# Optimization experiments

Measured on AMD Instinct MI355X. Metric: run time of the kernel, lower is better.

## Reference

```python
import jax, jax.numpy as jnp
import numpy as np

N, E, D_IN, H, L = 50000, 1_600_000, 3, 128, 4
MASK_RATIO = 0.15
GAMMA = 2.0
BN_EPS = 1e-5


def setup_inputs() -> dict:
    key = jax.random.key(0)
    ks = jax.random.split(key, 16)
    inp = {
        "x": jax.random.normal(ks[0], (N, D_IN), dtype=jnp.float32),
        "edge_index": jax.random.randint(ks[1], (2, E), 0, N, dtype=jnp.int32),
        "edge_attr": jax.random.normal(ks[2], (E, 4), dtype=jnp.float32),
        "mask": jax.random.uniform(ks[3], (N,)) < MASK_RATIO,
        # learned parameters
        "mask_token": 0.02 * jax.random.normal(ks[4], (D_IN,), dtype=jnp.float32),
        "embed_W": 0.1 * jax.random.normal(ks[5], (D_IN, H), dtype=jnp.float32),
        "embed_b": jnp.zeros((H,), dtype=jnp.float32),
        "conv_W1": 0.05 * jax.random.normal(ks[6], (L, H, 2 * H), dtype=jnp.float32),
        "conv_b1": jnp.zeros((L, 2 * H), dtype=jnp.float32),
        "conv_W2": 0.05 * jax.random.normal(ks[7], (L, 2 * H, H), dtype=jnp.float32),
        "conv_b2": jnp.zeros((L, H), dtype=jnp.float32),
        "bn_gamma": jnp.ones((L, H), dtype=jnp.float32),
        "bn_beta": jnp.zeros((L, H), dtype=jnp.float32),
        "dec_W1": 0.05 * jax.random.normal(ks[8], (H, H), dtype=jnp.float32),
        "dec_b1": jnp.zeros((H,), dtype=jnp.float32),
        "dec_W2": 0.05 * jax.random.normal(ks[9], (H, D_IN), dtype=jnp.float32),
        "dec_b2": jnp.zeros((D_IN,), dtype=jnp.float32),
    }
    return inp


def _l2norm(v):
    n = jnp.linalg.norm(v, axis=-1, keepdims=True)
    return v / jnp.maximum(n, 1e-12)


def reference(x, edge_index, edge_attr, mask, mask_token, embed_W, embed_b,
              conv_W1, conv_b1, conv_W2, conv_b2, bn_gamma, bn_beta,
              dec_W1, dec_b1, dec_W2, dec_b2):
    # --- masking: replace masked node features with learnable mask token ---
    masked_x = jnp.where(mask[:, None], mask_token[None, :], x)

    # --- GIN encoder ---
    h = masked_x @ embed_W + embed_b  # [N, H]
    src, dst = edge_index[0], edge_index[1]
    for l in range(L):
        # scatter-add aggregation: sum_{j in N(i)} h_j  (GINConv, eps=0)
        agg = jax.ops.segment_sum(h[src], dst, num_segments=N)  # [N, H]
        z = agg + h
        # MLP: H -> 2H -> H with ReLU
        z = jax.nn.relu(z @ conv_W1[l] + conv_b1[l]) @ conv_W2[l] + conv_b2[l]
        # BatchNorm1d (training-mode batch statistics, biased variance)
        mean = jnp.mean(z, axis=0)
        var = jnp.mean(jnp.square(z - mean), axis=0)
        z = (z - mean) * jax.lax.rsqrt(var + BN_EPS) * bn_gamma[l] + bn_beta[l]
        h = jax.nn.relu(z)  # dropout = identity (eval)

    # --- decoder: H -> H -> D_IN ---
    recon = jax.nn.relu(h @ dec_W1 + dec_b1) @ dec_W2 + dec_b2  # [N, D_IN]

    # --- scaled cosine error over masked nodes ---
    cos = jnp.sum(_l2norm(recon) * _l2norm(x), axis=-1)  # [N]
    per_node = jnp.power(1.0 - cos, GAMMA)
    m = mask.astype(recon.dtype)
    loss = jnp.sum(per_node * m) / jnp.maximum(jnp.sum(m), 1.0)
    return loss, recon
```

## Files before the change

### kernel.cpp

```cpp
#include <hip/hip_runtime.h>
#include <cstdint>

#define N_NODES 50000
#define N_EDGES 1600000
#define HDIM 128
#define L_LAYERS 4
#define BN_EPS 1e-5f
#define NPART 196
#define PART_SHIFT 8
#define PB_CHUNK 6250
#define FP_CAP 16384
#define FL_RB 128

typedef __attribute__((ext_vector_type(8))) short short8v;
typedef __attribute__((ext_vector_type(4))) float f32x4;

__device__ __forceinline__ unsigned short f2bf(float f) {
    uint32_t u = __builtin_bit_cast(uint32_t, f);
    u += 0x7fff + ((u >> 16) & 1);
    return (unsigned short)(u >> 16);
}
__device__ __forceinline__ float bf2f(unsigned short b) {
    return __builtin_bit_cast(float, (uint32_t)b << 16);
}

__global__ void detect_mask_kernel(const uint32_t* __restrict__ mw, int* __restrict__ flag) {
    __shared__ int f;
    if (threadIdx.x == 0) f = 0;
    __syncthreads();
    int found = 0;
    for (int i = threadIdx.x; i < 12500; i += blockDim.x)
        if (mw[i] > 1u) found = 1;
    if (found) f = 1;
    __syncthreads();
    if (threadIdx.x == 0) *flag = f;
}

__device__ __forceinline__ int read_mask(const void* mask, int i, int bytelayout) {
    if (bytelayout) return ((const unsigned char*)mask)[i] != 0;
    return ((const int*)mask)[i] != 0;
}

__global__ void wprep_all_kernel(const float* __restrict__ W1, const float* __restrict__ W2,
                                 const float* __restrict__ dW1, unsigned short* __restrict__ Wt1,
                                 unsigned short* __restrict__ Wt2,
                                 unsigned short* __restrict__ Wtd) {
    int seg = blockIdx.y;
    const float* W;
    unsigned short* Wt;
    int K, nshift;
    if (seg < 4) {
        W = W1 + (size_t)seg * HDIM * 2 * HDIM;
        Wt = Wt1 + (size_t)seg * HDIM * 2 * HDIM;
        K = HDIM;
        nshift = 8;
    } else if (seg < 8) {
        int l = seg - 4;
        W = W2 + (size_t)l * 2 * HDIM * HDIM;
        Wt = Wt2 + (size_t)l * 2 * HDIM * HDIM;
        K = 2 * HDIM;
        nshift = 7;
    } else {
        W = dW1;
        Wt = Wtd;
        K = HDIM;
        nshift = 7;
    }
    int total = K << nshift;
    for (int idx = blockIdx.x * 256 + threadIdx.x; idx < total; idx += gridDim.x * 256) {
        int k = idx >> nshift, n = idx & ((1 << nshift) - 1);
        Wt[(size_t)n * K + k] = f2bf(W[idx]);
    }
}

__global__ void embed_kernel(const float* __restrict__ x, const void* __restrict__ mask,
                             const int* __restrict__ flag, const float* __restrict__ tok,
                             const float* __restrict__ W, const float* __restrict__ b,
                             unsigned short* __restrict__ h) {
    int idx = blockIdx.x * blockDim.x + threadIdx.x;
    if (idx >= N_NODES * HDIM) return;
    int i = idx >> 7, c = idx & 127;
    int fl = *flag;
    int m = read_mask(mask, i, fl);
    float x0 = m ? tok[0] : x[i * 3 + 0];
    float x1 = m ? tok[1] : x[i * 3 + 1];
    float x2 = m ? tok[2] : x[i * 3 + 2];
    h[idx] = f2bf(x0 * W[c] + x1 * W[HDIM + c] + x2 * W[2 * HDIM + c] + b[c]);
}

__global__ __launch_bounds__(256) void pcount_kernel(const int* __restrict__ dst,
                                                     int* __restrict__ pcount) {
    __shared__ int hist[NPART];
    for (int i = threadIdx.x; i < NPART; i += 256) hist[i] = 0;
    __syncthreads();
    int lo = blockIdx.x * PB_CHUNK;
    for (int i = threadIdx.x; i < PB_CHUNK; i += 256)
        atomicAdd(&hist[dst[lo + i] >> PART_SHIFT], 1);
    __syncthreads();
    for (int i = threadIdx.x; i < NPART; i += 256)
        if (hist[i]) atomicAdd(&pcount[i], hist[i]);
}

__global__ __launch_bounds__(256) void pscan_kernel(const int* __restrict__ pcount,
                                                    int* __restrict__ poff,
                                                    int* __restrict__ pcursor,
                                                    int* __restrict__ rowptr) {
    __shared__ int sh[256];
    int t = threadIdx.x;
    int v = (t < NPART) ? pcount[t] : 0;
    sh[t] = v;
    __syncthreads();
    for (int o = 1; o < 256; o <<= 1) {
        int u = (t >= o) ? sh[t - o] : 0;
        __syncthreads();
        sh[t] += u;
        __syncthreads();
    }
    if (t < NPART) {
        int e = sh[t] - v;
        poff[t] = e;
        pcursor[t] = e;
    }
    if (t == NPART - 1) {
        poff[NPART] = sh[t];
        rowptr[N_NODES] = sh[t];
    }
}

__global__ __launch_bounds__(256) void partition_kernel(const int* __restrict__ src,
                                                        const int* __restrict__ dst,
                                                        int* __restrict__ pcursor,
                                                        uint32_t* __restrict__ pairs) {
    __shared__ int hist[NPART];
    __shared__ int off[NPART];
    int b = blockIdx.x, t = threadIdx.x;
    int lo = b * PB_CHUNK;
    for (int i = t; i < NPART; i += 256) hist[i] = 0;
    __syncthreads();
    for (int i = t; i < PB_CHUNK; i += 256) {
        int d = dst[lo + i];
        atomicAdd(&hist[d >> PART_SHIFT], 1);
    }
    __syncthreads();
    for (int i = t; i < NPART; i += 256) off[i] = atomicAdd(&pcursor[i], hist[i]);
    __syncthreads();
    for (int i = t; i < PB_CHUNK; i += 256) {
        int d = dst[lo + i];
        int s = src[lo + i];
        int pos = atomicAdd(&off[d >> PART_SHIFT], 1);
        pairs[pos] = (uint32_t)s | ((uint32_t)(d & 255) << 16);
    }
}

__global__ __launch_bounds__(256) void fill_part_kernel(const uint32_t* __restrict__ pairs,
                                                        const int* __restrict__ poff,
                                                        int* __restrict__ rowptr,
                                                        int* __restrict__ col) {
    __shared__ int colw[FP_CAP];
    __shared__ int lscan[256];
    __shared__ int lcur[256];
    int p = blockIdx.x, t = threadIdx.x;
    int base = p << PART_SHIFT;
    int nlocal = min(256, N_NODES - base);
    int pstart = poff[p], pend = poff[p + 1];
    int cnt = pend - pstart;
    lcur[t] = 0;
    __syncthreads();
    for (int e = pstart + t; e < pend; e += 256)
        atomicAdd(&lcur[(__builtin_nontemporal_load(&pairs[e]) >> 16) & 255], 1);
    __syncthreads();
    int v = lcur[t];
    lscan[t] = v;
    __syncthreads();
    for (int o = 1; o < 256; o <<= 1) {
        int u = (t >= o) ? lscan[t - o] : 0;
        __syncthreads();
        lscan[t] += u;
        __syncthreads();
    }
    int excl = lscan[t] - v;
    if (t < nlocal) rowptr[base + t] = pstart + excl;
    lcur[t] = excl;
    __syncthreads();
    if (cnt <= FP_CAP) {
        for (int e = pstart + t; e < pend; e += 256) {
            uint32_t pv = pairs[e];
            int pos = atomicAdd(&lcur[(pv >> 16) & 255], 1);
            colw[pos] = (int)(pv & 0xFFFFu);
        }
        __syncthreads();
        for (int e = t; e < cnt; e += 256) col[pstart + e] = colw[e];
    } else {
        for (int e = pstart + t; e < pend; e += 256) {
            uint32_t pv = pairs[e];
            int pos = atomicAdd(&lcur[(pv >> 16) & 255], 1);
            col[pstart + pos] = (int)(pv & 0xFFFFu);
        }
    }
}

__global__ __launch_bounds__(256) void agg_kernel(const unsigned short* __restrict__ h,
                                                  const int* __restrict__ rowptr,
                                                  const int* __restrict__ col,
                                                  unsigned short* __restrict__ z) {
    int wid = threadIdx.x >> 6;
    int lane = threadIdx.x & 63;
    int i = blockIdx.x * 4 + wid;
    if (i >= N_NODES) return;
    int start = rowptr[i], end = rowptr[i + 1];
    const uint32_t* h32 = (const uint32_t*)h;
    uint32_t u = h32[(size_t)i * 64 + lane];
    float ax = __builtin_bit_cast(float, u << 16);
    float ay = __builtin_bit_cast(float, u & 0xffff0000u);
    float bx = 0.f, by = 0.f, cx = 0.f, cy = 0.f, dx = 0.f, dy = 0.f;
    int e = start;
    for (; e + 4 <= end; e += 4) {
        int j0 = col[e + 0], j1 = col[e + 1], j2 = col[e + 2], j3 = col[e + 3];
        uint32_t u0 = h32[(size_t)j0 * 64 + lane];
        uint32_t u1 = h32[(size_t)j1 * 64 + lane];
        uint32_t u2 = h32[(size_t)j2 * 64 + lane];
        uint32_t u3 = h32[(size_t)j3 * 64 + lane];
        ax += __builtin_bit_cast(float, u0 << 16);
        ay += __builtin_bit_cast(float, u0 & 0xffff0000u);
        bx += __builtin_bit_cast(float, u1 << 16);
        by += __builtin_bit_cast(float, u1 & 0xffff0000u);
        cx += __builtin_bit_cast(float, u2 << 16);
        cy += __builtin_bit_cast(float, u2 & 0xffff0000u);
        dx += __builtin_bit_cast(float, u3 << 16);
        dy += __builtin_bit_cast(float, u3 & 0xffff0000u);
    }
    for (; e < end; ++e) {
        uint32_t u0 = h32[(size_t)col[e] * 64 + lane];
        ax += __builtin_bit_cast(float, u0 << 16);
        ay += __builtin_bit_cast(float, u0 & 0xffff0000u);
    }
    ax += bx + cx + dx;
    ay += by + cy + dy;
    uint32_t o = (uint32_t)f2bf(ax) | ((uint32_t)f2bf(ay) << 16);
    ((uint32_t*)z)[(size_t)i * 64 + lane] = o;
}

__global__ __launch_bounds__(512) void fused_layer_kernel(
    const unsigned short* __restrict__ z, const unsigned short* __restrict__ Wt1,
    const float* __restrict__ b1, const unsigned short* __restrict__ Wt2,
    const float* __restrict__ b2, float* __restrict__ zin, float* __restrict__ stats, int M) {
    __shared__ unsigned short wbuf[256 * 136];
    __shared__ unsigned short z1l[FL_RB * 264];
    const int t = threadIdx.x;
    const int lane = t & 63;
    const int w = t >> 6;
    const int r = lane & 15, ks = lane >> 4;
    const int row0 = blockIdx.x * FL_RB + w * 16;
    const int arow = min(row0 + r, M - 1);
    for (int i = t; i < 256 * 16; i += 512) {
        int row = i >> 4, seg = i & 15;
        *(short8v*)&wbuf[row * 136 + seg * 8] = *(const short8v*)&Wt1[(size_t)row * 128 + seg * 8];
    }
    short8v a4[4];
#pragma unroll
    for (int kk = 0; kk < 4; ++kk)
        a4[kk] = *(const short8v*)&z[(size_t)arow * HDIM + kk * 32 + ks * 8];
    __syncthreads();
#pragma unroll
    for (int n = 0; n < 16; ++n) {
        f32x4 acc = (f32x4){0.f, 0.f, 0.f, 0.f};
#pragma unroll
        for (int kk = 0; kk < 4; ++kk) {
            short8v bf = *(const short8v*)&wbuf[(n * 16 + r) * 136 + kk * 32 + ks * 8];
            acc = __builtin_amdgcn_mfma_f32_16x16x32_bf16(a4[kk], bf, acc, 0, 0, 0);
        }
        float bv = b1[n * 16 + r];
#pragma unroll
        for (int i = 0; i < 4; ++i) {
            float o = fmaxf(acc[i] + bv, 0.f);
            z1l[(w * 16 + ks * 4 + i) * 264 + n * 16 + r] = f2bf(o);
        }
    }
    __syncthreads();
    for (int i = t; i < 128 * 32; i += 512) {
        int row = i >> 5, seg = i & 31;
        *(short8v*)&wbuf[row * 264 + seg * 8] = *(const short8v*)&Wt2[(size_t)row * 256 + seg * 8];
    }
    __syncthreads();
    f32x4 accb[8];
#pragma unroll
    for (int n = 0; n < 8; ++n) accb[n] = (f32x4){0.f, 0.f, 0.f, 0.f};
#pragma unroll
    for (int k0 = 0; k0 < 256; k0 += 32) {
        short8v a = *(const short8v*)&z1l[(w * 16 + r) * 264 + k0 + ks * 8];
#pragma unroll
        for (int n = 0; n < 8; ++n) {
            short8v bf = *(const short8v*)&wbuf[(n * 16 + r) * 264 + k0 + ks * 8];
            accb[n] = __builtin_amdgcn_mfma_f32_16x16x32_bf16(a, bf, accb[n], 0, 0, 0);
        }
    }
    __syncthreads();
    float* sred = (float*)wbuf;
#pragma unroll
    for (int n = 0; n < 8; ++n) {
        const int cc = n * 16 + r;
        const float bv = b2[cc];
        float s = 0.f, ss = 0.f;
#pragma unroll
        for (int i = 0; i < 4; ++i) {
            int row = row0 + ks * 4 + i;
            if (row < M) {
                float o = accb[n][i] + bv;
                s += o;
                ss += o * o;
                zin[(size_t)row * HDIM + cc] = o;
            }
        }
        s += __shfl_xor(s, 16);
        s += __shfl_xor(s, 32);
        ss += __shfl_xor(ss, 16);
        ss += __shfl_xor(ss, 32);
        if (ks == 0) {
            sred[(w * 2 + 0) * HDIM + cc] = s;
            sred[(w * 2 + 1) * HDIM + cc] = ss;
        }
    }
    __syncthreads();
    if (t < HDIM) {
        float s = 0.f, ss = 0.f;
#pragma unroll
        for (int ww = 0; ww < 8; ++ww) {
            s += sred[(ww * 2 + 0) * HDIM + t];
            ss += sred[(ww * 2 + 1) * HDIM + t];
        }
        atomicAdd(&stats[t], s);
        atomicAdd(&stats[HDIM + t], ss);
    }
}

template <int K, bool OUT_BF16, bool RELU>
__global__ __launch_bounds__(256) void mfma_gemm_kernel(const unsigned short* __restrict__ A,
                                                        const unsigned short* __restrict__ Wt,
                                                        const float* __restrict__ bias,
                                                        void* __restrict__ C, int M, int ldc) {
    const int lane = threadIdx.x & 63;
    const int w = threadIdx.x >> 6;
    const int row0 = blockIdx.y * 64 + w * 16;
    const int col0 = blockIdx.x * 64;
    const int r = lane & 15;
    const int ks = lane >> 4;
    const int arow = min(row0 + r, M - 1);
    f32x4 acc[4];
#pragma unroll
    for (int n = 0; n < 4; ++n) acc[n] = (f32x4){0.f, 0.f, 0.f, 0.f};
#pragma unroll
    for (int k0 = 0; k0 < K; k0 += 32) {
        short8v a = *(const short8v*)&A[(size_t)arow * K + k0 + ks * 8];
#pragma unroll
        for (int n = 0; n < 4; ++n) {
            short8v b = *(const short8v*)&Wt[(size_t)(col0 + n * 16 + r) * K + k0 + ks * 8];
            acc[n] = __builtin_amdgcn_mfma_f32_16x16x32_bf16(a, b, acc[n], 0, 0, 0);
        }
    }
#pragma unroll
    for (int n = 0; n < 4; ++n) {
        const int col = col0 + n * 16 + r;
        const float bv = bias[col];
#pragma unroll
        for (int i = 0; i < 4; ++i) {
            int row = row0 + ks * 4 + i;
            if (row < M) {
                float o = acc[n][i] + bv;
                if (RELU) o = fmaxf(o, 0.f);
                if (OUT_BF16)
                    ((unsigned short*)C)[(size_t)row * ldc + col] = f2bf(o);
                else
                    ((float*)C)[(size_t)row * ldc + col] = o;
            }
        }
    }
}

__global__ void bnapply_kernel(const float* __restrict__ zin, const float* __restrict__ stats,
                               const float* __restrict__ gamma, const float* __restrict__ beta,
                               unsigned short* __restrict__ h) {
    __shared__ float ssc[2 * HDIM];
    int t = threadIdx.x;
    if (t < HDIM) {
        float mean = stats[t] * (1.f / N_NODES);
        float var = stats[HDIM + t] * (1.f / N_NODES) - mean * mean;
        float rstd = rsqrtf(fmaxf(var, 0.f) + BN_EPS);
        float s = gamma[t] * rstd;
        ssc[t] = s;
        ssc[HDIM + t] = beta[t] - mean * s;
    }
    __syncthreads();
    int idx = blockIdx.x * blockDim.x + threadIdx.x;
    if (idx >= N_NODES * HDIM / 4) return;
    float4 v = ((const float4*)zin)[idx];
    int c = (idx * 4) & 127;
    float o0 = fmaxf(v.x * ssc[c + 0] + ssc[HDIM + c + 0], 0.f);
    float o1 = fmaxf(v.y * ssc[c + 1] + ssc[HDIM + c + 1], 0.f);
    float o2 = fmaxf(v.z * ssc[c + 2] + ssc[HDIM + c + 2], 0.f);
    float o3 = fmaxf(v.w * ssc[c + 3] + ssc[HDIM + c + 3], 0.f);
    uint2 p;
    p.x = (uint32_t)f2bf(o0) | ((uint32_t)f2bf(o1) << 16);
    p.y = (uint32_t)f2bf(o2) | ((uint32_t)f2bf(o3) << 16);
    ((uint2*)h)[idx] = p;
}

__global__ __launch_bounds__(256) void dec2_loss_kernel(
    const unsigned short* __restrict__ d1, const float* __restrict__ W2,
    const float* __restrict__ b2, const float* __restrict__ x, const void* __restrict__ mask,
    const int* __restrict__ flag, float* __restrict__ recon, float* __restrict__ acc) {
    __shared__ float w2s[HDIM * 3];
    for (int t = threadIdx.x; t < HDIM * 3; t += 256) w2s[t] = W2[t];
    __syncthreads();
    int i = blockIdx.x * 256 + threadIdx.x;
    int fl = *flag;
    float lsum = 0.f, lcnt = 0.f;
    if (i < N_NODES) {
        float s0 = 0.f, s1 = 0.f, s2 = 0.f;
        const unsigned short* row = &d1[(size_t)i * HDIM];
#pragma unroll
        for (int k0 = 0; k0 < HDIM; k0 += 8) {
            short8v v = *(const short8v*)&row[k0];
#pragma unroll
            for (int q = 0; q < 8; ++q) {
                float a = bf2f((unsigned short)v[q]);
                s0 = fmaf(a, w2s[(k0 + q) * 3 + 0], s0);
                s1 = fmaf(a, w2s[(k0 + q) * 3 + 1], s1);
                s2 = fmaf(a, w2s[(k0 + q) * 3 + 2], s2);
            }
        }
        float r0 = s0 + b2[0], r1 = s1 + b2[1], r2 = s2 + b2[2];
        recon[(size_t)i * 3 + 0] = r0;
        recon[(size_t)i * 3 + 1] = r1;
        recon[(size_t)i * 3 + 2] = r2;
        if (read_mask(mask, i, fl)) {
            float rn = fmaxf(sqrtf(r0 * r0 + r1 * r1 + r2 * r2), 1e-12f);
            float x0 = x[i * 3 + 0], x1 = x[i * 3 + 1], x2 = x[i * 3 + 2];
            float xn = fmaxf(sqrtf(x0 * x0 + x1 * x1 + x2 * x2), 1e-12f);
            float cs = (r0 * x0 + r1 * x1 + r2 * x2) / (rn * xn);
            float d = 1.f - cs;
            lsum = d * d;
            lcnt = 1.f;
        }
    }
#pragma unroll
    for (int o = 32; o > 0; o >>= 1) {
        lsum += __shfl_xor(lsum, o);
        lcnt += __shfl_xor(lcnt, o);
    }
    if ((threadIdx.x & 63) == 0 && lcnt != 0.f) {
        atomicAdd(&acc[0], lsum);
        atomicAdd(&acc[1], lcnt);
    }
}

__global__ void finalize_kernel(const float* __restrict__ acc, float* __restrict__ out) {
    out[0] = acc[0] / fmaxf(acc[1], 1.f);
}

extern "C" void kernel_launch(void* const* d_in, const int* in_sizes, int n_in, void* d_out,
                              int out_size, void* d_ws, size_t ws_size, hipStream_t stream) {
    const float* x = (const float*)d_in[0];
    const int* ei = (const int*)d_in[1];
    const int* src = ei;
    const int* dst = ei + N_EDGES;
    const void* mask = d_in[3];
    const float* tok = (const float*)d_in[4];
    const float* eW = (const float*)d_in[5];
    const float* eb = (const float*)d_in[6];
    const float* W1 = (const float*)d_in[7];
    const float* b1 = (const float*)d_in[8];
    const float* W2 = (const float*)d_in[9];
    const float* b2 = (const float*)d_in[10];
    const float* gm = (const float*)d_in[11];
    const float* bt = (const float*)d_in[12];
    const float* dW1 = (const float*)d_in[13];
    const float* db1 = (const float*)d_in[14];
    const float* dW2 = (const float*)d_in[15];
    const float* db2 = (const float*)d_in[16];
    float* out = (float*)d_out;

    char* ws = (char*)d_ws;
    size_t off = 0;
    auto alloc = [&](size_t bytes) -> void* {
        void* p = ws + off;
        off = (off + bytes + 255) & ~(size_t)255;
        return p;
    };
    unsigned short* h = (unsigned short*)alloc((size_t)N_NODES * HDIM * 2);
    unsigned short* z = (unsigned short*)alloc((size_t)N_NODES * HDIM * 2);
    unsigned short* z1 = (unsigned short*)alloc((size_t)N_NODES * 2 * HDIM * 2);
    float* zin = (float*)alloc((size_t)N_NODES * HDIM * 4);
    unsigned short* Wt1 = (unsigned short*)alloc((size_t)L_LAYERS * HDIM * 2 * HDIM * 2);
    unsigned short* Wt2 = (unsigned short*)alloc((size_t)L_LAYERS * HDIM * 2 * HDIM * 2);
    unsigned short* Wtd = (unsigned short*)alloc((size_t)HDIM * HDIM * 2);
    int* rowptr = (int*)alloc((size_t)(N_NODES + 1) * 4);
    int* col = (int*)alloc((size_t)N_EDGES * 4);
    uint32_t* pairs = (uint32_t*)alloc((size_t)N_EDGES * 4);
    int* pcount = (int*)alloc((size_t)NPART * 4);
    int* poff = (int*)alloc((size_t)(NPART + 1) * 4);
    int* pcursor = (int*)alloc((size_t)NPART * 4);
    float* stats = (float*)alloc((size_t)L_LAYERS * 2 * HDIM * 4);
    float* lacc = (float*)alloc(8);
    int* flag = (int*)alloc(4);

    detect_mask_kernel<<<1, 256, 0, stream>>>((const uint32_t*)mask, flag);
    wprep_all_kernel<<<dim3(32, 9), 256, 0, stream>>>(W1, W2, dW1, Wt1, Wt2, Wtd);
    embed_kernel<<<(N_NODES * HDIM + 255) / 256, 256, 0, stream>>>(x, mask, flag, tok, eW, eb, h);

    hipMemsetAsync(pcount, 0, (size_t)NPART * 4, stream);
    hipMemsetAsync(stats, 0, (size_t)L_LAYERS * 2 * HDIM * 4, stream);
    hipMemsetAsync(lacc, 0, 8, stream);
    pcount_kernel<<<256, 256, 0, stream>>>(dst, pcount);
    pscan_kernel<<<1, 256, 0, stream>>>(pcount, poff, pcursor, rowptr);
    partition_kernel<<<256, 256, 0, stream>>>(src, dst, pcursor, pairs);
    fill_part_kernel<<<NPART, 256, 0, stream>>>(pairs, poff, rowptr, col);

    for (int l = 0; l < L_LAYERS; ++l) {
        float* lstats = stats + (size_t)l * 2 * HDIM;
        agg_kernel<<<(N_NODES + 3) / 4, 256, 0, stream>>>(h, rowptr, col, z);
        fused_layer_kernel<<<(N_NODES + FL_RB - 1) / FL_RB, 512, 0, stream>>>(
            z, Wt1 + (size_t)l * HDIM * 2 * HDIM, b1 + (size_t)l * 2 * HDIM,
            Wt2 + (size_t)l * HDIM * 2 * HDIM, b2 + (size_t)l * HDIM, zin, lstats, N_NODES);
        bnapply_kernel<<<(N_NODES * HDIM / 4 + 255) / 256, 256, 0, stream>>>(
            zin, lstats, gm + l * HDIM, bt + l * HDIM, h);
    }

    mfma_gemm_kernel<HDIM, true, true><<<dim3(2, 782), 256, 0, stream>>>(h, Wtd, db1, z1, N_NODES,
                                                                         HDIM);
    dec2_loss_kernel<<<(N_NODES + 255) / 256, 256, 0, stream>>>(z1, dW2, db2, x, mask, flag,
                                                                out + 1, lacc);
    finalize_kernel<<<1, 1, 0, stream>>>(lacc, out);
}
```

Baseline: 542.2 us.

## Merge setup kernels, consolidate memsets, widen aggregation unroll, fold loss finalize

```diff
diff --git a/kernel.cpp b/kernel.cpp
--- a/kernel.cpp
+++ b/kernel.cpp
@@ -24,60 +24,74 @@
     return __builtin_bit_cast(float, (uint32_t)b << 16);
 }
 
-__global__ void detect_mask_kernel(const uint32_t* __restrict__ mw, int* __restrict__ flag) {
-    __shared__ int f;
-    if (threadIdx.x == 0) f = 0;
-    __syncthreads();
-    int found = 0;
-    for (int i = threadIdx.x; i < 12500; i += blockDim.x)
-        if (mw[i] > 1u) found = 1;
-    if (found) f = 1;
-    __syncthreads();
-    if (threadIdx.x == 0) *flag = f;
-}
-
 __device__ __forceinline__ int read_mask(const void* mask, int i, int bytelayout) {
     if (bytelayout) return ((const unsigned char*)mask)[i] != 0;
     return ((const int*)mask)[i] != 0;
 }
 
-__global__ void wprep_all_kernel(const float* __restrict__ W1, const float* __restrict__ W2,
-                                 const float* __restrict__ dW1, unsigned short* __restrict__ Wt1,
-                                 unsigned short* __restrict__ Wt2,
-                                 unsigned short* __restrict__ Wtd) {
-    int seg = blockIdx.y;
-    const float* W;
-    unsigned short* Wt;
-    int K, nshift;
-    if (seg < 4) {
-        W = W1 + (size_t)seg * HDIM * 2 * HDIM;
-        Wt = Wt1 + (size_t)seg * HDIM * 2 * HDIM;
-        K = HDIM;
-        nshift = 8;
-    } else if (seg < 8) {
-        int l = seg - 4;
-        W = W2 + (size_t)l * 2 * HDIM * HDIM;
-        Wt = Wt2 + (size_t)l * 2 * HDIM * HDIM;
-        K = 2 * HDIM;
-        nshift = 7;
-    } else {
-        W = dW1;
-        Wt = Wtd;
-        K = HDIM;
-        nshift = 7;
-    }
-    int total = K << nshift;
-    for (int idx = blockIdx.x * 256 + threadIdx.x; idx < total; idx += gridDim.x * 256) {
-        int k = idx >> nshift, n = idx & ((1 << nshift) - 1);
-        Wt[(size_t)n * K + k] = f2bf(W[idx]);
-    }
-}
-
-__global__ void embed_kernel(const float* __restrict__ x, const void* __restrict__ mask,
-                             const int* __restrict__ flag, const float* __restrict__ tok,
-                             const float* __restrict__ W, const float* __restrict__ b,
-                             unsigned short* __restrict__ h) {
-    int idx = blockIdx.x * blockDim.x + threadIdx.x;
+__global__ __launch_bounds__(256) void detect_pcount_kernel(const uint32_t* __restrict__ mw,
+                                                            int* __restrict__ flag,
+                                                            const int* __restrict__ dst,
+                                                            int* __restrict__ pcount) {
+    if (blockIdx.x == 256) {
+        __shared__ int f;
+        if (threadIdx.x == 0) f = 0;
+        __syncthreads();
+        int found = 0;
+        for (int i = threadIdx.x; i < 12500; i += 256)
+            if (mw[i] > 1u) found = 1;
+        if (found) f = 1;
+        __syncthreads();
+        if (threadIdx.x == 0) *flag = f;
+        return;
+    }
+    __shared__ int hist[NPART];
+    for (int i = threadIdx.x; i < NPART; i += 256) hist[i] = 0;
+    __syncthreads();
+    int lo = blockIdx.x * PB_CHUNK;
+    for (int i = threadIdx.x; i < PB_CHUNK; i += 256)
+        atomicAdd(&hist[dst[lo + i] >> PART_SHIFT], 1);
+    __syncthreads();
+    for (int i = threadIdx.x; i < NPART; i += 256)
+        if (hist[i]) atomicAdd(&pcount[i], hist[i]);
+}
+
+__global__ __launch_bounds__(256) void wprep_embed_kernel(
+    const float* __restrict__ W1, const float* __restrict__ W2, const float* __restrict__ dW1,
+    unsigned short* __restrict__ Wt1, unsigned short* __restrict__ Wt2,
+    unsigned short* __restrict__ Wtd, const float* __restrict__ x, const void* __restrict__ mask,
+    const int* __restrict__ flag, const float* __restrict__ tok, const float* __restrict__ eW,
+    const float* __restrict__ eb, unsigned short* __restrict__ h) {
+    if (blockIdx.x < 288) {
+        int seg = blockIdx.x / 32, bx = blockIdx.x & 31;
+        const float* W;
+        unsigned short* Wt;
+        int K, nshift;
+        if (seg < 4) {
+            W = W1 + (size_t)seg * HDIM * 2 * HDIM;
+            Wt = Wt1 + (size_t)seg * HDIM * 2 * HDIM;
+            K = HDIM;
+            nshift = 8;
+        } else if (seg < 8) {
+            int l = seg - 4;
+            W = W2 + (size_t)l * 2 * HDIM * HDIM;
+            Wt = Wt2 + (size_t)l * 2 * HDIM * HDIM;
+            K = 2 * HDIM;
+            nshift = 7;
+        } else {
+            W = dW1;
+            Wt = Wtd;
+            K = HDIM;
+            nshift = 7;
+        }
+        int total = K << nshift;
+        for (int idx = bx * 256 + (int)threadIdx.x; idx < total; idx += 32 * 256) {
+            int k = idx >> nshift, n = idx & ((1 << nshift) - 1);
+            Wt[(size_t)n * K + k] = f2bf(W[idx]);
+        }
+        return;
+    }
+    int idx = (blockIdx.x - 288) * 256 + threadIdx.x;
     if (idx >= N_NODES * HDIM) return;
     int i = idx >> 7, c = idx & 127;
     int fl = *flag;
@@ -85,20 +99,7 @@
     float x0 = m ? tok[0] : x[i * 3 + 0];
     float x1 = m ? tok[1] : x[i * 3 + 1];
     float x2 = m ? tok[2] : x[i * 3 + 2];
-    h[idx] = f2bf(x0 * W[c] + x1 * W[HDIM + c] + x2 * W[2 * HDIM + c] + b[c]);
-}
-
-__global__ __launch_bounds__(256) void pcount_kernel(const int* __restrict__ dst,
-                                                     int* __restrict__ pcount) {
-    __shared__ int hist[NPART];
-    for (int i = threadIdx.x; i < NPART; i += 256) hist[i] = 0;
-    __syncthreads();
-    int lo = blockIdx.x * PB_CHUNK;
-    for (int i = threadIdx.x; i < PB_CHUNK; i += 256)
-        atomicAdd(&hist[dst[lo + i] >> PART_SHIFT], 1);
-    __syncthreads();
-    for (int i = threadIdx.x; i < NPART; i += 256)
-        if (hist[i]) atomicAdd(&pcount[i], hist[i]);
+    h[idx] = f2bf(x0 * eW[c] + x1 * eW[HDIM + c] + x2 * eW[2 * HDIM + c] + eb[c]);
 }
 
 __global__ __launch_bounds__(256) void pscan_kernel(const int* __restrict__ pcount,
@@ -199,44 +200,54 @@
     }
 }
 
+#define AGG_LD(k)                                        \
+    {                                                    \
+        uint32_t uu = h32[(size_t)j##k * 64 + lane];     \
+        ac##k.x += __builtin_bit_cast(float, uu << 16);  \
+        ac##k.y += __builtin_bit_cast(float, uu & 0xffff0000u); \
+    }
 __global__ __launch_bounds__(256) void agg_kernel(const unsigned short* __restrict__ h,
                                                   const int* __restrict__ rowptr,
                                                   const int* __restrict__ col,
                                                   unsigned short* __restrict__ z) {
     int wid = threadIdx.x >> 6;
     int lane = threadIdx.x & 63;
-    int i = blockIdx.x * 4 + wid;
+    int i = __builtin_amdgcn_readfirstlane(blockIdx.x * 4 + wid);
     if (i >= N_NODES) return;
     int start = rowptr[i], end = rowptr[i + 1];
     const uint32_t* h32 = (const uint32_t*)h;
     uint32_t u = h32[(size_t)i * 64 + lane];
-    float ax = __builtin_bit_cast(float, u << 16);
-    float ay = __builtin_bit_cast(float, u & 0xffff0000u);
-    float bx = 0.f, by = 0.f, cx = 0.f, cy = 0.f, dx = 0.f, dy = 0.f;
+    float2 ac0 = make_float2(__builtin_bit_cast(float, u << 16),
+                             __builtin_bit_cast(float, u & 0xffff0000u));
+    float2 ac1 = make_float2(0.f, 0.f), ac2 = make_float2(0.f, 0.f), ac3 = make_float2(0.f, 0.f);
+    float2 ac4 = make_float2(0.f, 0.f), ac5 = make_float2(0.f, 0.f), ac6 = make_float2(0.f, 0.f);
+    float2 ac7 = make_float2(0.f, 0.f), ac8 = make_float2(0.f, 0.f), ac9 = make_float2(0.f, 0.f);
+    float2 ac10 = make_float2(0.f, 0.f), ac11 = make_float2(0.f, 0.f),
+           ac12 = make_float2(0.f, 0.f);
+    float2 ac13 = make_float2(0.f, 0.f), ac14 = make_float2(0.f, 0.f),
+           ac15 = make_float2(0.f, 0.f);
     int e = start;
+    for (; e + 16 <= end; e += 16) {
+        int j0 = col[e + 0], j1 = col[e + 1], j2 = col[e + 2], j3 = col[e + 3];
+        int j4 = col[e + 4], j5 = col[e + 5], j6 = col[e + 6], j7 = col[e + 7];
+        int j8 = col[e + 8], j9 = col[e + 9], j10 = col[e + 10], j11 = col[e + 11];
+        int j12 = col[e + 12], j13 = col[e + 13], j14 = col[e + 14], j15 = col[e + 15];
+        AGG_LD(0) AGG_LD(1) AGG_LD(2) AGG_LD(3) AGG_LD(4) AGG_LD(5) AGG_LD(6) AGG_LD(7)
+        AGG_LD(8) AGG_LD(9) AGG_LD(10) AGG_LD(11) AGG_LD(12) AGG_LD(13) AGG_LD(14) AGG_LD(15)
+    }
     for (; e + 4 <= end; e += 4) {
         int j0 = col[e + 0], j1 = col[e + 1], j2 = col[e + 2], j3 = col[e + 3];
-        uint32_t u0 = h32[(size_t)j0 * 64 + lane];
-        uint32_t u1 = h32[(size_t)j1 * 64 + lane];
-        uint32_t u2 = h32[(size_t)j2 * 64 + lane];
-        uint32_t u3 = h32[(size_t)j3 * 64 + lane];
-        ax += __builtin_bit_cast(float, u0 << 16);
-        ay += __builtin_bit_cast(float, u0 & 0xffff0000u);
-        bx += __builtin_bit_cast(float, u1 << 16);
-        by += __builtin_bit_cast(float, u1 & 0xffff0000u);
-        cx += __builtin_bit_cast(float, u2 << 16);
-        cy += __builtin_bit_cast(float, u2 & 0xffff0000u);
-        dx += __builtin_bit_cast(float, u3 << 16);
-        dy += __builtin_bit_cast(float, u3 & 0xffff0000u);
+        AGG_LD(0) AGG_LD(1) AGG_LD(2) AGG_LD(3)
     }
     for (; e < end; ++e) {
-        uint32_t u0 = h32[(size_t)col[e] * 64 + lane];
-        ax += __builtin_bit_cast(float, u0 << 16);
-        ay += __builtin_bit_cast(float, u0 & 0xffff0000u);
-    }
-    ax += bx + cx + dx;
-    ay += by + cy + dy;
-    uint32_t o = (uint32_t)f2bf(ax) | ((uint32_t)f2bf(ay) << 16);
+        int j0 = col[e];
+        AGG_LD(0)
+    }
+    ac0.x += ((ac1.x + ac2.x) + (ac3.x + ac4.x)) + ((ac5.x + ac6.x) + (ac7.x + ac8.x)) +
+             ((ac9.x + ac10.x) + (ac11.x + ac12.x)) + ((ac13.x + ac14.x) + ac15.x);
+    ac0.y += ((ac1.y + ac2.y) + (ac3.y + ac4.y)) + ((ac5.y + ac6.y) + (ac7.y + ac8.y)) +
+             ((ac9.y + ac10.y) + (ac11.y + ac12.y)) + ((ac13.y + ac14.y) + ac15.y);
+    uint32_t o = (uint32_t)f2bf(ac0.x) | ((uint32_t)f2bf(ac0.y) << 16);
     ((uint32_t*)z)[(size_t)i * 64 + lane] = o;
 }
 
@@ -407,7 +418,8 @@
 __global__ __launch_bounds__(256) void dec2_loss_kernel(
     const unsigned short* __restrict__ d1, const float* __restrict__ W2,
     const float* __restrict__ b2, const float* __restrict__ x, const void* __restrict__ mask,
-    const int* __restrict__ flag, float* __restrict__ recon, float* __restrict__ acc) {
+    const int* __restrict__ flag, float* __restrict__ recon, float* __restrict__ acc,
+    int* __restrict__ cnt, float* __restrict__ out_loss, int nblocks) {
     __shared__ float w2s[HDIM * 3];
     for (int t = threadIdx.x; t < HDIM * 3; t += 256) w2s[t] = W2[t];
     __syncthreads();
@@ -451,10 +463,15 @@
         atomicAdd(&acc[0], lsum);
         atomicAdd(&acc[1], lcnt);
     }
-}
-
-__global__ void finalize_kernel(const float* __restrict__ acc, float* __restrict__ out) {
-    out[0] = acc[0] / fmaxf(acc[1], 1.f);
+    __syncthreads();
+    if (threadIdx.x == 0) {
+        __threadfence();
+        int done = atomicAdd(cnt, 1);
+        if (done == nblocks - 1) {
+            __threadfence();
+            out_loss[0] = acc[0] / fmaxf(acc[1], 1.f);
+        }
+    }
 }
 
 extern "C" void kernel_launch(void* const* d_in, const int* in_sizes, int n_in, void* d_out,
@@ -496,21 +513,20 @@
     int* rowptr = (int*)alloc((size_t)(N_NODES + 1) * 4);
     int* col = (int*)alloc((size_t)N_EDGES * 4);
     uint32_t* pairs = (uint32_t*)alloc((size_t)N_EDGES * 4);
-    int* pcount = (int*)alloc((size_t)NPART * 4);
     int* poff = (int*)alloc((size_t)(NPART + 1) * 4);
     int* pcursor = (int*)alloc((size_t)NPART * 4);
+    int* flag = (int*)alloc(4);
+    char* zr0 = ws + off;
+    int* pcount = (int*)alloc((size_t)NPART * 4);
     float* stats = (float*)alloc((size_t)L_LAYERS * 2 * HDIM * 4);
     float* lacc = (float*)alloc(8);
-    int* flag = (int*)alloc(4);
-
-    detect_mask_kernel<<<1, 256, 0, stream>>>((const uint32_t*)mask, flag);
-    wprep_all_kernel<<<dim3(32, 9), 256, 0, stream>>>(W1, W2, dW1, Wt1, Wt2, Wtd);
-    embed_kernel<<<(N_NODES * HDIM + 255) / 256, 256, 0, stream>>>(x, mask, flag, tok, eW, eb, h);
-
-    hipMemsetAsync(pcount, 0, (size_t)NPART * 4, stream);
-    hipMemsetAsync(stats, 0, (size_t)L_LAYERS * 2 * HDIM * 4, stream);
-    hipMemsetAsync(lacc, 0, 8, stream);
-    pcount_kernel<<<256, 256, 0, stream>>>(dst, pcount);
+    int* cnt = (int*)alloc(4);
+    size_t zr_bytes = (ws + off) - zr0;
+
+    hipMemsetAsync(zr0, 0, zr_bytes, stream);
+    detect_pcount_kernel<<<257, 256, 0, stream>>>((const uint32_t*)mask, flag, dst, pcount);
+    wprep_embed_kernel<<<288 + (N_NODES * HDIM + 255) / 256, 256, 0, stream>>>(
+        W1, W2, dW1, Wt1, Wt2, Wtd, x, mask, flag, tok, eW, eb, h);
     pscan_kernel<<<1, 256, 0, stream>>>(pcount, poff, pcursor, rowptr);
     partition_kernel<<<256, 256, 0, stream>>>(src, dst, pcursor, pairs);
     fill_part_kernel<<<NPART, 256, 0, stream>>>(pairs, poff, rowptr, col);
@@ -527,7 +543,7 @@
 
     mfma_gemm_kernel<HDIM, true, true><<<dim3(2, 782), 256, 0, stream>>>(h, Wtd, db1, z1, N_NODES,
                                                                          HDIM);
-    dec2_loss_kernel<<<(N_NODES + 255) / 256, 256, 0, stream>>>(z1, dW2, db2, x, mask, flag,
-                                                                out + 1, lacc);
-    finalize_kernel<<<1, 1, 0, stream>>>(lacc, out);
-}
+    const int D2B = (N_NODES + 255) / 256;
+    dec2_loss_kernel<<<D2B, 256, 0, stream>>>(z1, dW2, db2, x, mask, flag, out + 1, lacc, cnt, out,
+                                              D2B);
+}
```

After: 481.0 us. -11.3%, faster.
